# Performance work log

Measured on AMD Instinct MI355X. Metric: run time of the kernel, lower is better.

## Reference

```python
import jax, jax.numpy as jnp
import numpy as np

N = 100000
E = 3200000
D = 256
HOPS = 3  # K + 1


def setup_inputs() -> dict:
    key = jax.random.key(0)
    k1, k2, k3, k4, k5 = jax.random.split(key, 5)
    node_features = jax.random.normal(k1, (N, D), dtype=jnp.float32)
    # glorot-uniform-like scale for K+1 Dense kernels
    limit = np.sqrt(6.0 / (D + D)).astype(np.float32)
    W = jax.random.uniform(k2, (HOPS, D, D), dtype=jnp.float32, minval=-limit, maxval=limit)
    adj_vals = jax.random.uniform(k3, (HOPS, E), dtype=jnp.float32)
    adj_rows = jax.random.randint(k4, (HOPS, E), 0, N, dtype=jnp.int32)
    adj_cols = jax.random.randint(k5, (HOPS, E), 0, N, dtype=jnp.int32)
    return {"node_features": node_features, "W": W, "adj_vals": adj_vals,
            "adj_rows": adj_rows, "adj_cols": adj_cols}


def reference(node_features, W, adj_vals, adj_rows, adj_cols):
    """Faithful eval-mode forward: sum over hops of SpMM(A_hop, X @ W_hop), then ReLU.
    Dropout is identity at inference (training=False)."""
    n = node_features.shape[0]
    out = jnp.zeros((n, W.shape[-1]), dtype=node_features.dtype)
    for hop in range(W.shape[0]):  # small fixed K+1 loop, structurally distinct hops
        feats = node_features @ W[hop]                      # [N, out_dim]
        msgs = adj_vals[hop][:, None] * feats[adj_cols[hop]]  # gather + scale, [E, out_dim]
        out = out + jax.ops.segment_sum(msgs, adj_rows[hop], num_segments=n)
    return jax.nn.relu(out)
```

## Files before the change

kernel.cpp:

```cpp
#include <hip/hip_runtime.h>

#define D 256
#define MAXB 512
#define PCH 32768

typedef __attribute__((ext_vector_type(8))) short short8;
typedef __attribute__((ext_vector_type(4))) float f32x4;

__device__ __forceinline__ ushort f2b(float f) {
    unsigned u = __float_as_uint(f);
    u += 0x7fffu + ((u >> 16) & 1u);
    return (ushort)(u >> 16);
}
__device__ __forceinline__ float b2f(ushort h) {
    return __uint_as_float(((unsigned)h) << 16);
}
__device__ __forceinline__ long long ntload_ll(const void* p) {
    return __builtin_nontemporal_load((const long long*)p);
}

__global__ void zero_int_kernel(int* __restrict__ p, int n) {
    int stride = gridDim.x * blockDim.x;
    for (int i = blockIdx.x * blockDim.x + threadIdx.x; i < n; i += stride) p[i] = 0;
}

__global__ void xconv_kernel(const float* __restrict__ X, ushort* __restrict__ Xb, int total8) {
    int i = blockIdx.x * 256 + threadIdx.x;
    if (i >= total8) return;
    const float4 a = *(const float4*)(X + (size_t)i * 8);
    const float4 b = *(const float4*)(X + (size_t)i * 8 + 4);
    ushort o8[8] = {f2b(a.x), f2b(a.y), f2b(a.z), f2b(a.w),
                    f2b(b.x), f2b(b.y), f2b(b.z), f2b(b.w)};
    *(short8*)(Xb + (size_t)i * 8) = *(const short8*)o8;
}

__global__ void wconv_kernel(const float* __restrict__ W, ushort* __restrict__ WT, int total) {
    int idx = blockIdx.x * 256 + threadIdx.x;
    if (idx >= total) return;
    int h = idx >> 16;
    int c = (idx >> 8) & 255, k = idx & 255;
    WT[(h << 16) + c * 256 + k] = f2b(W[(h << 16) + k * 256 + c]);
}

__global__ __launch_bounds__(256) void bhist_kernel(const int* __restrict__ rows,
                                                    int* __restrict__ bhistG, int e, int nbuk) {
    __shared__ int lh[MAXB];
    int h = blockIdx.y;
    const int* r = rows + (size_t)h * e;
    for (int k = threadIdx.x; k < nbuk; k += 256) lh[k] = 0;
    __syncthreads();
    int stride = gridDim.x * 256;
    for (int i = blockIdx.x * 256 + threadIdx.x; i < e; i += stride)
        atomicAdd(&lh[r[i] >> 8], 1);
    __syncthreads();
    int* g = bhistG + (size_t)h * nbuk;
    for (int k = threadIdx.x; k < nbuk; k += 256)
        if (lh[k]) atomicAdd(&g[k], lh[k]);
}

__global__ __launch_bounds__(1024) void bscan_kernel(const int* __restrict__ bhistG,
                                                     int* __restrict__ gbase,
                                                     int* __restrict__ gcur, int total) {
    __shared__ int s[1024];
    int t = threadIdx.x;
    int C = (total + 1023) >> 10;
    int i0 = t * C, i1 = min(i0 + C, total);
    int sum = 0;
    for (int i = i0; i < i1; ++i) sum += bhistG[i];
    s[t] = sum;
    __syncthreads();
    for (int off = 1; off < 1024; off <<= 1) {
        int x = (t >= off) ? s[t - off] : 0;
        __syncthreads();
        s[t] += x;
        __syncthreads();
    }
    int run = s[t] - sum;
    for (int i = i0; i < i1; ++i) {
        gbase[i] = run; gcur[i] = run;
        run += bhistG[i];
    }
    if (t == 1023) gbase[total] = s[1023];
}

__global__ __launch_bounds__(256) void bpart_kernel(const int* __restrict__ rows,
                                                    const int* __restrict__ cols,
                                                    const float* __restrict__ vals,
                                                    int* __restrict__ gcur, int2* __restrict__ raw,
                                                    int e, int nbuk) {
    __shared__ int lbase[MAXB];
    __shared__ int lcur[MAXB];
    int h = blockIdx.y;
    const int*   rr = rows + (size_t)h * e;
    const int*   cc = cols + (size_t)h * e;
    const float* vv = vals + (size_t)h * e;
    int c0 = blockIdx.x * PCH;
    int c1 = min(c0 + PCH, e);
    if (c0 >= c1) return;
    for (int k = threadIdx.x; k < nbuk; k += 256) { lbase[k] = 0; lcur[k] = 0; }
    __syncthreads();
    for (int i = c0 + threadIdx.x; i < c1; i += 256)
        atomicAdd(&lbase[rr[i] >> 8], 1);
    __syncthreads();
    int* gc = gcur + (size_t)h * nbuk;
    for (int k = threadIdx.x; k < nbuk; k += 256) {
        int c = lbase[k];
        lbase[k] = c ? atomicAdd(&gc[k], c) : 0;
    }
    __syncthreads();
    for (int i = c0 + threadIdx.x; i < c1; i += 256) {
        int row = rr[i];
        int b = row >> 8;
        int p = lbase[b] + atomicAdd(&lcur[b], 1);
        raw[p] = make_int2(cc[i] | ((row & 255) << 17), __float_as_int(vv[i]));
    }
}

__global__ __launch_bounds__(256) void bsort_kernel(const int* __restrict__ gbase,
                                                    const int2* __restrict__ raw,
                                                    int2* __restrict__ eg,
                                                    int* __restrict__ row_ptr,
                                                    int n, int nbuk) {
    __shared__ int hist[256], ss[256], cur[256];
    int key = blockIdx.x;
    int h = key / nbuk, b = key % nbuk;
    int s = gbase[key], t = gbase[key + 1];
    int tid = threadIdx.x;
    hist[tid] = 0;
    __syncthreads();
    for (int i = s + tid; i < t; i += 256)
        atomicAdd(&hist[(((unsigned)raw[i].x) >> 17) & 255], 1);
    __syncthreads();
    int v = hist[tid];
    ss[tid] = v;
    __syncthreads();
    for (int off = 1; off < 256; off <<= 1) {
        int x = (tid >= off) ? ss[tid - off] : 0;
        __syncthreads();
        ss[tid] += x;
        __syncthreads();
    }
    int excl = s + ss[tid] - v;
    cur[tid] = excl;
    int* rp = row_ptr + (size_t)h * (n + 1);
    int grow = b * 256 + tid;
    if (grow < n) rp[grow] = excl;
    if (tid == 255 && b == nbuk - 1) rp[n] = t;
    __syncthreads();
    for (int i = s + tid; i < t; i += 256) {
        int2 ev = raw[i];
        int j = (((unsigned)ev.x) >> 17) & 255;
        int p = atomicAdd(&cur[j], 1);
        eg[p] = ev;
    }
}

__global__ __launch_bounds__(256) void spmmX_kernel(const int* __restrict__ rp,
                                                    const int2* __restrict__ eg,
                                                    const ushort* __restrict__ Xb,
                                                    ushort* __restrict__ Yh, int n) {
    int w = threadIdx.x >> 6, lane = threadIdx.x & 63;
    int r = blockIdx.x * 4 + w;
    if (r >= n) return;
    int half = lane >> 5, l5 = lane & 31;
    int doff = l5 * 8;
    int e0 = rp[r], e1 = rp[r + 1];
    float acc[8] = {};
    int m0 = e0 + half, m1 = e0 + 2 + half;
    long long ev0 = (m0 < e1) ? ntload_ll(eg + m0) : 0;
    long long ev1 = (m1 < e1) ? ntload_ll(eg + m1) : 0;
    for (int ee = e0; ee < e1; ee += 4) {
        long long c0 = ev0, c1 = ev1;
        int n0 = ee + 4 + half, n1 = ee + 6 + half;
        ev0 = (n0 < e1) ? ntload_ll(eg + n0) : 0;
        ev1 = (n1 < e1) ? ntload_ll(eg + n1) : 0;
        int col0 = ((int)(unsigned)c0) & 0x1FFFF;
        int col1 = ((int)(unsigned)c1) & 0x1FFFF;
        short8 v0 = *(const short8*)(Xb + (size_t)col0 * 256 + doff);
        short8 v1 = *(const short8*)(Xb + (size_t)col1 * 256 + doff);
        float val0 = __int_as_float((int)(c0 >> 32));
        float val1 = __int_as_float((int)(c1 >> 32));
        #pragma unroll
        for (int i = 0; i < 8; ++i)
            acc[i] = fmaf(val0, b2f((ushort)v0[i]), acc[i]);
        #pragma unroll
        for (int i = 0; i < 8; ++i)
            acc[i] = fmaf(val1, b2f((ushort)v1[i]), acc[i]);
    }
    #pragma unroll
    for (int i = 0; i < 8; ++i)
        acc[i] += __shfl_xor(acc[i], 32);
    if (half == 0) {
        union { ushort u[8]; long long ll[2]; } o;
        #pragma unroll
        for (int i = 0; i < 8; ++i) o.u[i] = f2b(acc[i]);
        long long* dst = (long long*)(Yh + (size_t)r * 256 + doff);
        __builtin_nontemporal_store(o.ll[0], dst);
        __builtin_nontemporal_store(o.ll[1], dst + 1);
    }
}

#define APAD 40

__global__ __launch_bounds__(256) void gemmY_kernel(const ushort* __restrict__ Y,
                                                    const ushort* __restrict__ WT,
                                                    float* __restrict__ out, int M,
                                                    int nh, int mode) {
    __shared__ ushort As[64 * APAD];
    __shared__ ushort Bs[64 * APAD];
    int tid = threadIdx.x;
    int r0 = blockIdx.x * 64, c0 = blockIdx.y * 64;
    int w = tid >> 6, lane = tid & 63;
    int wr = w >> 1, wc = w & 1;
    int lo = lane & 15, hi = lane >> 4;
    f32x4 acc[2][2] = {};
    int srow = tid >> 2;
    int skoff = (tid & 3) * 8;
    int arow = r0 + srow; if (arow > M - 1) arow = M - 1;
    for (int h = 0; h < nh; ++h) {
        const ushort* ap = Y + ((size_t)h * M + arow) * 256 + skoff;
        const ushort* bp = WT + ((size_t)h << 16) + (size_t)(c0 + srow) * 256 + skoff;
        for (int kk = 0; kk < 256; kk += 32) {
            short8 av = *(const short8*)(ap + kk);
            short8 bv = *(const short8*)(bp + kk);
            __syncthreads();
            *(short8*)&As[srow * APAD + skoff] = av;
            *(short8*)&Bs[srow * APAD + skoff] = bv;
            __syncthreads();
            short8 a0 = *(const short8*)&As[(wr * 32 +      lo) * APAD + hi * 8];
            short8 a1 = *(const short8*)&As[(wr * 32 + 16 + lo) * APAD + hi * 8];
            short8 b0 = *(const short8*)&Bs[(wc * 32 +      lo) * APAD + hi * 8];
            short8 b1 = *(const short8*)&Bs[(wc * 32 + 16 + lo) * APAD + hi * 8];
            acc[0][0] = __builtin_amdgcn_mfma_f32_16x16x32_bf16(a0, b0, acc[0][0], 0, 0, 0);
            acc[0][1] = __builtin_amdgcn_mfma_f32_16x16x32_bf16(a0, b1, acc[0][1], 0, 0, 0);
            acc[1][0] = __builtin_amdgcn_mfma_f32_16x16x32_bf16(a1, b0, acc[1][0], 0, 0, 0);
            acc[1][1] = __builtin_amdgcn_mfma_f32_16x16x32_bf16(a1, b1, acc[1][1], 0, 0, 0);
        }
    }
    for (int mi = 0; mi < 2; ++mi)
        for (int ni = 0; ni < 2; ++ni)
            for (int i = 0; i < 4; ++i) {
                int row = r0 + wr * 32 + mi * 16 + hi * 4 + i;
                int col = c0 + wc * 32 + ni * 16 + lo;
                if (row < M) {
                    float v = acc[mi][ni][i];
                    float* op = &out[(size_t)row * 256 + col];
                    if (mode & 1) v += *op;
                    if (mode & 2) v = fmaxf(v, 0.f);
                    *op = v;
                }
            }
}

extern "C" void kernel_launch(void* const* d_in, const int* in_sizes, int n_in,
                              void* d_out, int out_size, void* d_ws, size_t ws_size,
                              hipStream_t stream) {
    const float* X    = (const float*)d_in[0];
    const float* W    = (const float*)d_in[1];
    const float* vals = (const float*)d_in[2];
    const int*   rows = (const int*)d_in[3];
    const int*   cols = (const int*)d_in[4];
    int n    = in_sizes[0] / D;
    int hops = in_sizes[1] / (D * D);
    int e    = in_sizes[2] / hops;

    int nbuk    = (n + 255) / 256;
    int nkeytot = hops * nbuk;
    int nchunks = (e + PCH - 1) / PCH;

    float* out = (float*)d_out;

    auto padded = [](size_t b) { return (b + 255) & ~(size_t)255; };
    char* wsb = (char*)d_ws;
    size_t off = 0;
    auto alloc = [&](size_t bytes) -> void* { void* p = wsb + off; off += padded(bytes); return p; };

    ushort* WT      = (ushort*)alloc((size_t)hops * D * D * 2);
    ushort* Xb      = (ushort*)alloc((size_t)n * D * 2);
    int*    bhistG  = (int*)   alloc((size_t)nkeytot * 4);
    int*    gbase   = (int*)   alloc((size_t)(nkeytot + 1) * 4);
    int*    gcur    = (int*)   alloc((size_t)nkeytot * 4);
    int*    row_ptr = (int*)   alloc((size_t)hops * (n + 1) * 4);
    int2*   edges   = (int2*)  alloc((size_t)hops * e * 8);
    size_t  raw_off = off;
    int2*   raw     = (int2*)  alloc((size_t)hops * e * 8);

    bool bigY = (ws_size >= raw_off + (size_t)hops * n * D * 2);
    ushort* Y = (ushort*)raw;

    xconv_kernel<<<(n * D / 8 + 255) / 256, 256, 0, stream>>>(X, Xb, n * D / 8);
    wconv_kernel<<<(hops * D * D + 255) / 256, 256, 0, stream>>>(W, WT, hops * D * D);

    zero_int_kernel<<<(nkeytot + 255) / 256, 256, 0, stream>>>(bhistG, nkeytot);
    bhist_kernel<<<dim3(128, hops), 256, 0, stream>>>(rows, bhistG, e, nbuk);
    bscan_kernel<<<1, 1024, 0, stream>>>(bhistG, gbase, gcur, nkeytot);
    bpart_kernel<<<dim3(nchunks, hops), 256, 0, stream>>>(rows, cols, vals, gcur, raw, e, nbuk);
    bsort_kernel<<<nkeytot, 256, 0, stream>>>(gbase, raw, edges, row_ptr, n, nbuk);

    if (bigY) {
        for (int h = 0; h < hops; ++h)
            spmmX_kernel<<<(n + 3) / 4, 256, 0, stream>>>(row_ptr + (size_t)h * (n + 1), edges,
                                                          Xb, Y + (size_t)h * n * D, n);
        gemmY_kernel<<<dim3((n + 63) / 64, D / 64), 256, 0, stream>>>(Y, WT, out, n, hops, 2);
    } else {
        for (int h = 0; h < hops; ++h) {
            spmmX_kernel<<<(n + 3) / 4, 256, 0, stream>>>(row_ptr + (size_t)h * (n + 1), edges,
                                                          Xb, Y, n);
            int mode = (h > 0 ? 1 : 0) | (h == hops - 1 ? 2 : 0);
            gemmY_kernel<<<dim3((n + 63) / 64, D / 64), 256, 0, stream>>>(Y, WT + (size_t)h * D * D,
                                                                          out, n, 1, mode);
        }
    }
}
```

Measured before the change: 1.193 ms.

## Use 1024-row buckets for edge sort and widen SpMM lanes to 16 features

The bucketed counting sort now groups rows into buckets of 1024 instead of 256. That cuts the bucket count, the global atomics and the partition scatter targets, and bpart and bsort run with 512 threads. The bsort scan now handles two rows per thread. Each SpMM lane now loads 16 bf16 features instead of 8, and 4 lane groups process different edges with a software-pipelined gather of the next edge's X row. The cost is higher register use, larger shared histograms, and an extra cross-lane shuffle reduction step.

```diff
diff --git a/kernel.cpp b/kernel.cpp
--- a/kernel.cpp
+++ b/kernel.cpp
@@ -1,8 +1,8 @@
 #include <hip/hip_runtime.h>
 
 #define D 256
-#define MAXB 512
-#define PCH 32768
+#define MAXB 128
+#define PCH 16384
 
 typedef __attribute__((ext_vector_type(8))) short short8;
 typedef __attribute__((ext_vector_type(4))) float f32x4;
@@ -51,7 +51,7 @@
     __syncthreads();
     int stride = gridDim.x * 256;
     for (int i = blockIdx.x * 256 + threadIdx.x; i < e; i += stride)
-        atomicAdd(&lh[r[i] >> 8], 1);
+        atomicAdd(&lh[r[i] >> 10], 1);
     __syncthreads();
     int* g = bhistG + (size_t)h * nbuk;
     for (int k = threadIdx.x; k < nbuk; k += 256)
@@ -83,7 +83,7 @@
     if (t == 1023) gbase[total] = s[1023];
 }
 
-__global__ __launch_bounds__(256) void bpart_kernel(const int* __restrict__ rows,
+__global__ __launch_bounds__(512) void bpart_kernel(const int* __restrict__ rows,
                                                     const int* __restrict__ cols,
                                                     const float* __restrict__ vals,
                                                     int* __restrict__ gcur, int2* __restrict__ raw,
@@ -97,59 +97,64 @@
     int c0 = blockIdx.x * PCH;
     int c1 = min(c0 + PCH, e);
     if (c0 >= c1) return;
-    for (int k = threadIdx.x; k < nbuk; k += 256) { lbase[k] = 0; lcur[k] = 0; }
-    __syncthreads();
-    for (int i = c0 + threadIdx.x; i < c1; i += 256)
-        atomicAdd(&lbase[rr[i] >> 8], 1);
+    for (int k = threadIdx.x; k < nbuk; k += 512) { lbase[k] = 0; lcur[k] = 0; }
+    __syncthreads();
+    for (int i = c0 + threadIdx.x; i < c1; i += 512)
+        atomicAdd(&lbase[rr[i] >> 10], 1);
     __syncthreads();
     int* gc = gcur + (size_t)h * nbuk;
-    for (int k = threadIdx.x; k < nbuk; k += 256) {
+    for (int k = threadIdx.x; k < nbuk; k += 512) {
         int c = lbase[k];
         lbase[k] = c ? atomicAdd(&gc[k], c) : 0;
     }
     __syncthreads();
-    for (int i = c0 + threadIdx.x; i < c1; i += 256) {
+    for (int i = c0 + threadIdx.x; i < c1; i += 512) {
         int row = rr[i];
-        int b = row >> 8;
+        int b = row >> 10;
         int p = lbase[b] + atomicAdd(&lcur[b], 1);
-        raw[p] = make_int2(cc[i] | ((row & 255) << 17), __float_as_int(vv[i]));
-    }
-}
-
-__global__ __launch_bounds__(256) void bsort_kernel(const int* __restrict__ gbase,
+        raw[p] = make_int2(cc[i] | ((row & 1023) << 17), __float_as_int(vv[i]));
+    }
+}
+
+__global__ __launch_bounds__(512) void bsort_kernel(const int* __restrict__ gbase,
                                                     const int2* __restrict__ raw,
                                                     int2* __restrict__ eg,
                                                     int* __restrict__ row_ptr,
                                                     int n, int nbuk) {
-    __shared__ int hist[256], ss[256], cur[256];
+    __shared__ int hist[1024];
+    __shared__ int ss[512];
+    __shared__ int cur[1024];
     int key = blockIdx.x;
     int h = key / nbuk, b = key % nbuk;
     int s = gbase[key], t = gbase[key + 1];
     int tid = threadIdx.x;
-    hist[tid] = 0;
-    __syncthreads();
-    for (int i = s + tid; i < t; i += 256)
-        atomicAdd(&hist[(((unsigned)raw[i].x) >> 17) & 255], 1);
-    __syncthreads();
-    int v = hist[tid];
-    ss[tid] = v;
-    __syncthreads();
-    for (int off = 1; off < 256; off <<= 1) {
+    hist[tid] = 0; hist[tid + 512] = 0;
+    __syncthreads();
+    for (int i = s + tid; i < t; i += 512)
+        atomicAdd(&hist[(((unsigned)raw[i].x) >> 17) & 1023], 1);
+    __syncthreads();
+    int a = hist[2 * tid], c = hist[2 * tid + 1];
+    int pair = a + c;
+    ss[tid] = pair;
+    __syncthreads();
+    for (int off = 1; off < 512; off <<= 1) {
         int x = (tid >= off) ? ss[tid - off] : 0;
         __syncthreads();
         ss[tid] += x;
         __syncthreads();
     }
-    int excl = s + ss[tid] - v;
-    cur[tid] = excl;
+    int excl = s + ss[tid] - pair;
+    cur[2 * tid] = excl;
+    cur[2 * tid + 1] = excl + a;
     int* rp = row_ptr + (size_t)h * (n + 1);
-    int grow = b * 256 + tid;
-    if (grow < n) rp[grow] = excl;
-    if (tid == 255 && b == nbuk - 1) rp[n] = t;
-    __syncthreads();
-    for (int i = s + tid; i < t; i += 256) {
+    int grow = b * 1024 + 2 * tid;
+    if (grow < n)     rp[grow]     = excl;
+    if (grow + 1 < n) rp[grow + 1] = excl + a;
+    if (tid == 511 && b == nbuk - 1) rp[n] = t;
+    __syncthreads();
+    for (int i = s + tid; i < t; i += 512) {
         int2 ev = raw[i];
-        int j = (((unsigned)ev.x) >> 17) & 255;
+        int j = (((unsigned)ev.x) >> 17) & 1023;
         int p = atomicAdd(&cur[j], 1);
         eg[p] = ev;
     }
@@ -162,41 +167,50 @@
     int w = threadIdx.x >> 6, lane = threadIdx.x & 63;
     int r = blockIdx.x * 4 + w;
     if (r >= n) return;
-    int half = lane >> 5, l5 = lane & 31;
-    int doff = l5 * 8;
+    int g = lane >> 4, l4 = lane & 15;
+    int doff = l4 * 16;
+    const ushort* xb = Xb + doff;
     int e0 = rp[r], e1 = rp[r + 1];
-    float acc[8] = {};
-    int m0 = e0 + half, m1 = e0 + 2 + half;
-    long long ev0 = (m0 < e1) ? ntload_ll(eg + m0) : 0;
-    long long ev1 = (m1 < e1) ? ntload_ll(eg + m1) : 0;
+    float acc[16] = {};
+
+    int i0 = e0 + g;
+    long long d_cur = (i0 < e1) ? ntload_ll(eg + i0) : 0;
+    int c_cur = ((int)(unsigned)d_cur) & 0x1FFFF;
+    short8 va = *(const short8*)(xb + (size_t)c_cur * 256);
+    short8 vb = *(const short8*)(xb + (size_t)c_cur * 256 + 8);
+    int i1 = e0 + 4 + g;
+    long long d_nxt = (i1 < e1) ? ntload_ll(eg + i1) : 0;
+
     for (int ee = e0; ee < e1; ee += 4) {
-        long long c0 = ev0, c1 = ev1;
-        int n0 = ee + 4 + half, n1 = ee + 6 + half;
-        ev0 = (n0 < e1) ? ntload_ll(eg + n0) : 0;
-        ev1 = (n1 < e1) ? ntload_ll(eg + n1) : 0;
-        int col0 = ((int)(unsigned)c0) & 0x1FFFF;
-        int col1 = ((int)(unsigned)c1) & 0x1FFFF;
-        short8 v0 = *(const short8*)(Xb + (size_t)col0 * 256 + doff);
-        short8 v1 = *(const short8*)(Xb + (size_t)col1 * 256 + doff);
-        float val0 = __int_as_float((int)(c0 >> 32));
-        float val1 = __int_as_float((int)(c1 >> 32));
+        int c_nxt = ((int)(unsigned)d_nxt) & 0x1FFFF;
+        short8 wa = *(const short8*)(xb + (size_t)c_nxt * 256);
+        short8 wb = *(const short8*)(xb + (size_t)c_nxt * 256 + 8);
+        int i2 = ee + 8 + g;
+        long long d_n2 = (i2 < e1) ? ntload_ll(eg + i2) : 0;
+
+        float val = __int_as_float((int)(d_cur >> 32));
         #pragma unroll
         for (int i = 0; i < 8; ++i)
-            acc[i] = fmaf(val0, b2f((ushort)v0[i]), acc[i]);
+            acc[i] = fmaf(val, b2f((ushort)va[i]), acc[i]);
         #pragma unroll
         for (int i = 0; i < 8; ++i)
-            acc[i] = fmaf(val1, b2f((ushort)v1[i]), acc[i]);
+            acc[8 + i] = fmaf(val, b2f((ushort)vb[i]), acc[8 + i]);
+
+        d_cur = d_nxt; va = wa; vb = wb; d_nxt = d_n2;
     }
     #pragma unroll
-    for (int i = 0; i < 8; ++i)
-        acc[i] += __shfl_xor(acc[i], 32);
-    if (half == 0) {
-        union { ushort u[8]; long long ll[2]; } o;
+    for (int i = 0; i < 16; ++i) acc[i] += __shfl_xor(acc[i], 16);
+    #pragma unroll
+    for (int i = 0; i < 16; ++i) acc[i] += __shfl_xor(acc[i], 32);
+    if (g == 0) {
+        union { ushort u[16]; long long ll[4]; } o;
         #pragma unroll
-        for (int i = 0; i < 8; ++i) o.u[i] = f2b(acc[i]);
+        for (int i = 0; i < 16; ++i) o.u[i] = f2b(acc[i]);
         long long* dst = (long long*)(Yh + (size_t)r * 256 + doff);
         __builtin_nontemporal_store(o.ll[0], dst);
         __builtin_nontemporal_store(o.ll[1], dst + 1);
+        __builtin_nontemporal_store(o.ll[2], dst + 2);
+        __builtin_nontemporal_store(o.ll[3], dst + 3);
     }
 }
 
@@ -264,7 +278,7 @@
     int hops = in_sizes[1] / (D * D);
     int e    = in_sizes[2] / hops;
 
-    int nbuk    = (n + 255) / 256;
+    int nbuk    = (n + 1023) / 1024;
     int nkeytot = hops * nbuk;
     int nchunks = (e + PCH - 1) / PCH;
 
@@ -294,8 +308,8 @@
     zero_int_kernel<<<(nkeytot + 255) / 256, 256, 0, stream>>>(bhistG, nkeytot);
     bhist_kernel<<<dim3(128, hops), 256, 0, stream>>>(rows, bhistG, e, nbuk);
     bscan_kernel<<<1, 1024, 0, stream>>>(bhistG, gbase, gcur, nkeytot);
-    bpart_kernel<<<dim3(nchunks, hops), 256, 0, stream>>>(rows, cols, vals, gcur, raw, e, nbuk);
-    bsort_kernel<<<nkeytot, 256, 0, stream>>>(gbase, raw, edges, row_ptr, n, nbuk);
+    bpart_kernel<<<dim3(nchunks, hops), 512, 0, stream>>>(rows, cols, vals, gcur, raw, e, nbuk);
+    bsort_kernel<<<nkeytot, 512, 0, stream>>>(gbase, raw, edges, row_ptr, n, nbuk);
 
     if (bigY) {
         for (int h = 0; h < hops; ++h)
```

Measured after the change: 1.136 ms. 1.05x faster.
